# Optimization experiments

Hardware: AMD Instinct MI355X
Metric: run time of the kernel (lower is better)

The kernel has to match this reference:

```python
import jax, jax.numpy as jnp
import numpy as np

N = 16384   # nodes
D = 64      # feature dim
K = 20      # neighbors (self.k)
CHUNK = 2048  # row tile size (mirrors KeOps tiling; avoids n x n materialization)


def setup_inputs() -> dict:
    key = jax.random.key(0)
    k1, = jax.random.split(key, 1)
    x = jax.random.normal(k1, (N, D), dtype=jnp.float32)
    A = jnp.zeros((1,), dtype=jnp.int32)  # unused: embed_f is identity
    temperature = jnp.asarray(4.0, dtype=jnp.float32)  # nn.Parameter init for euclidean
    return {"x": x, "A": A, "temperature": temperature}


def reference(x, A, temperature):
    # embed_f = identity -> x stays [n, d]; batch dim b=1 added at the end
    n, d = x.shape
    scale = jnp.exp(jnp.clip(temperature, -5.0, 5.0))
    sq = jnp.sum(x * x, axis=-1)  # [n]

    def chunk_knn(xc):  # xc: [CHUNK, d]
        # squared euclidean distances of chunk rows vs all points: [CHUNK, n]
        d2 = jnp.sum(xc * xc, axis=-1, keepdims=True) + sq[None, :] - 2.0 * (xc @ x.T)
        # argKmin over j of d2 * scale  (scale > 0 so ordering matches original)
        _, idx = jax.lax.top_k(-(d2 * scale), K)
        return idx  # [CHUNK, K]

    idx = jax.lax.map(chunk_knn, x.reshape(n // CHUNK, CHUNK, d)).reshape(n, K)

    # gather neighbors and recompute logprobs exactly as the torch gather path
    x1 = x[idx]                                  # [n, K, d]
    d2 = jnp.sum((x1 - x[:, None, :]) ** 2, -1)  # [n, K]
    logprobs = (-d2 * scale)[None]               # [1, n, K]

    rows = jnp.broadcast_to(jnp.arange(n)[:, None], (n, K)).reshape(-1)
    # sparse=True, b=1: offset arange(b)*n == 0, final shape [2, b*n*k]
    edges = jnp.stack((idx.reshape(-1), rows), axis=0)  # [2, n*K]

    return (x[None], edges, logprobs)
```

## Files before the change

kernel.cpp:

```cpp
#include <hip/hip_runtime.h>
#include <math.h>

#define NN 16384
#define DD 64
#define KK 20
#define SAMP_CH 16
#define SAMP_PER 32
#define SAMP_N 512
#define THR_EPS 1e-3f
#define BF16_MARGIN 0.25f
#define FCH 4
#define SLOTS 128
#define CAP2 512
#define GS 2

#define SCALE_ULP_NUDGE (+1)

typedef __attribute__((ext_vector_type(8)))  short bf16x8;
typedef __attribute__((ext_vector_type(16))) float f32x16;

__device__ __forceinline__ float nudge_ulp(float v, int n) {
    return __uint_as_float(__float_as_uint(v) + (unsigned)n);
}

__device__ __forceinline__ unsigned short f2bf(float f) {
    unsigned u = __float_as_uint(f);
    return (unsigned short)((u + 0x7fffu + ((u >> 16) & 1u)) >> 16);
}

__device__ __forceinline__ unsigned ordmap(float f) {
    unsigned u = __float_as_uint(f);
    return u ^ ((u & 0x80000000u) ? 0xFFFFFFFFu : 0x80000000u);
}

__device__ __forceinline__ float fast_key(const float* __restrict__ xj4,
                                          const float* xi, float sqj) {
    const float4* xj = reinterpret_cast<const float4*>(xj4);
    float c0 = 0.f, c1 = 0.f, c2 = 0.f, c3 = 0.f;
#pragma unroll
    for (int q = 0; q < 16; ++q) {
        float4 v = xj[q];
        c0 = fmaf(xi[4 * q + 0], v.x, c0);
        c1 = fmaf(xi[4 * q + 1], v.y, c1);
        c2 = fmaf(xi[4 * q + 2], v.z, c2);
        c3 = fmaf(xi[4 * q + 3], v.w, c3);
    }
    return sqj - 2.0f * ((c0 + c1) + (c2 + c3));
}

__device__ __forceinline__ float ref_key(const float* __restrict__ xj4,
                                         const float* xi, float sqi, float sqj,
                                         float scale) {
    const float4* xj = reinterpret_cast<const float4*>(xj4);
    float c = 0.0f;
#pragma unroll
    for (int q = 0; q < 16; ++q) {
        float4 v = xj[q];
        c = fmaf(xi[4 * q + 0], v.x, c);
        c = fmaf(xi[4 * q + 1], v.y, c);
        c = fmaf(xi[4 * q + 2], v.z, c);
        c = fmaf(xi[4 * q + 3], v.w, c);
    }
    float t1 = sqi + sqj;
    float d2 = fmaf(-2.0f, c, t1);
    return d2 * scale;
}

__device__ __forceinline__ float gather_d2(const float* xi,
                                           const float* __restrict__ xj4) {
#pragma clang fp contract(off)
    const float4* xn = reinterpret_cast<const float4*>(xj4);
    float r0, r1, r2, r3, r4, r5, r6, r7;
    {
        float4 v0 = xn[0], v1 = xn[1];
        float d0 = xi[0] - v0.x, d1 = xi[1] - v0.y, d2 = xi[2] - v0.z, d3 = xi[3] - v0.w;
        float d4 = xi[4] - v1.x, d5 = xi[5] - v1.y, d6 = xi[6] - v1.z, d7 = xi[7] - v1.w;
        r0 = d0 * d0; r1 = d1 * d1; r2 = d2 * d2; r3 = d3 * d3;
        r4 = d4 * d4; r5 = d5 * d5; r6 = d6 * d6; r7 = d7 * d7;
    }
#pragma unroll
    for (int t = 1; t < 8; ++t) {
        float4 v0 = xn[2 * t], v1 = xn[2 * t + 1];
        float d0 = xi[8 * t + 0] - v0.x, d1 = xi[8 * t + 1] - v0.y;
        float d2 = xi[8 * t + 2] - v0.z, d3 = xi[8 * t + 3] - v0.w;
        float d4 = xi[8 * t + 4] - v1.x, d5 = xi[8 * t + 5] - v1.y;
        float d6 = xi[8 * t + 6] - v1.z, d7 = xi[8 * t + 7] - v1.w;
        r0 += d0 * d0; r1 += d1 * d1; r2 += d2 * d2; r3 += d3 * d3;
        r4 += d4 * d4; r5 += d5 * d5; r6 += d6 * d6; r7 += d7 * d7;
    }
    return ((r0 + r1) + (r2 + r3)) + ((r4 + r5) + (r6 + r7));
}

__global__ __launch_bounds__(256) void copy_x_kernel(const float* __restrict__ x,
                                                     float* __restrict__ out_x,
                                                     unsigned short* __restrict__ xb) {
    int t = blockIdx.x * blockDim.x + threadIdx.x;
    float4 v = reinterpret_cast<const float4*>(x)[t];
    reinterpret_cast<float4*>(out_x)[t] = v;
    ushort4 w;
    w.x = f2bf(v.x); w.y = f2bf(v.y); w.z = f2bf(v.z); w.w = f2bf(v.w);
    reinterpret_cast<ushort4*>(xb)[t] = w;
}

__global__ __launch_bounds__(256, 2) void sq_kernel(const float* __restrict__ x,
                                                    float* __restrict__ sq) {
#pragma clang fp contract(off)
    int r = blockIdx.x * blockDim.x + threadIdx.x;
    const float4* p = reinterpret_cast<const float4*>(x + (size_t)r * DD);
    float r0, r1, r2, r3, r4, r5, r6, r7;
    {
        float4 v0 = p[0], v1 = p[1];
        r0 = v0.x * v0.x; r1 = v0.y * v0.y; r2 = v0.z * v0.z; r3 = v0.w * v0.w;
        r4 = v1.x * v1.x; r5 = v1.y * v1.y; r6 = v1.z * v1.z; r7 = v1.w * v1.w;
    }
#pragma unroll
    for (int t = 1; t < 8; ++t) {
        float4 v0 = p[2 * t], v1 = p[2 * t + 1];
        r0 += v0.x * v0.x; r1 += v0.y * v0.y; r2 += v0.z * v0.z; r3 += v0.w * v0.w;
        r4 += v1.x * v1.x; r5 += v1.y * v1.y; r6 += v1.z * v1.z; r7 += v1.w * v1.w;
    }
    sq[r] = ((r0 + r1) + (r2 + r3)) + ((r4 + r5) + (r6 + r7));
}

__global__ __launch_bounds__(256, 2) void sample_kernel(const float* __restrict__ x,
                                                        const float* __restrict__ sq,
                                                        float* __restrict__ psum,
                                                        float* __restrict__ psumsq) {
    int g = blockIdx.x * blockDim.x + threadIdx.x;
    int i = g & (NN - 1);
    int c = g >> 14;

    float xi[DD];
#pragma unroll
    for (int d = 0; d < DD; d += 4) {
        float4 v = *reinterpret_cast<const float4*>(x + (size_t)i * DD + d);
        xi[d + 0] = v.x; xi[d + 1] = v.y; xi[d + 2] = v.z; xi[d + 3] = v.w;
    }

    float s = 0.0f, ss = 0.0f;
#pragma unroll 2
    for (int t = 0; t < SAMP_PER; ++t) {
        int j = ((c * SAMP_PER + t) << 5);
        float key = fast_key(x + (size_t)j * DD, xi, sq[j]);
        s += key;
        ss = fmaf(key, key, ss);
    }
    psum[i * SAMP_CH + c]   = s;
    psumsq[i * SAMP_CH + c] = ss;
}

__global__ __launch_bounds__(256) void thr_kernel(const float* __restrict__ psum,
                                                  const float* __restrict__ psumsq,
                                                  const float* __restrict__ sq,
                                                  float* __restrict__ thr) {
    int i = blockIdx.x * blockDim.x + threadIdx.x;
    float S = 0.0f, SS = 0.0f;
#pragma unroll
    for (int c = 0; c < SAMP_CH; ++c) {
        S  += psum[i * SAMP_CH + c];
        SS += psumsq[i * SAMP_CH + c];
    }
    float mean = S * (1.0f / SAMP_N);
    float var  = fmaxf(SS * (1.0f / SAMP_N) - mean * mean, 1.0f);
    float sig  = sqrtf(var);
    float sqi  = sq[i];
    float t2   = 2.0f * (64.0f + 2.0f * sqi);
    float gam  = 8.0f * (64.0f + 3.0f * sqi) / (t2 * sqrtf(t2));
    const float zt = 2.25f;
    float zeff = zt - gam * (zt * zt - 1.0f) * (1.0f / 6.0f);
    thr[i] = mean - zeff * sig + THR_EPS;
}

__global__ __launch_bounds__(256, 2) void filter_mfma_kernel(
    const unsigned short* __restrict__ xb, const float* __restrict__ sq,
    const float* __restrict__ thr, unsigned short* __restrict__ cnt2d,
    unsigned short* __restrict__ surv2d) {
    __shared__ __align__(16) unsigned short lbuf[32][SLOTS];
    __shared__ int lcnt[32];

    const int wave = threadIdx.x >> 6;
    const int lane = threadIdx.x & 63;
    const int bi = blockIdx.x >> 2;
    const int bj = blockIdx.x & 3;
    const int i0 = bi * 32;
    const int jw0 = bj * 4096 + wave * 1024;

    const int arow = i0 + (lane & 31);
    const int koff = (lane >> 5) * 8;

    bf16x8 a[4];
#pragma unroll
    for (int q = 0; q < 4; ++q)
        a[q] = *reinterpret_cast<const bf16x8*>(xb + (size_t)arow * DD + koff + 16 * q);

    float thrv[16];
#pragma unroll
    for (int r = 0; r < 16; ++r) {
        int row = i0 + (r & 3) + 8 * (r >> 2) + 4 * (lane >> 5);
        thrv[r] = thr[row] + BF16_MARGIN;
    }

    if (threadIdx.x < 32) lcnt[threadIdx.x] = 0;
    __syncthreads();

    for (int t = 0; t < 32; ++t) {
        const int j0 = jw0 + t * 32;
        const int jcol = j0 + (lane & 31);
        bf16x8 b[4];
#pragma unroll
        for (int q = 0; q < 4; ++q)
            b[q] = *reinterpret_cast<const bf16x8*>(xb + (size_t)jcol * DD + koff + 16 * q);

        f32x16 acc;
#pragma unroll
        for (int r = 0; r < 16; ++r) acc[r] = 0.0f;
#pragma unroll
        for (int q = 0; q < 4; ++q)
            acc = __builtin_amdgcn_mfma_f32_32x32x16_bf16(a[q], b[q], acc, 0, 0, 0);

        const float sqj = sq[jcol];
#pragma unroll
        for (int r = 0; r < 16; ++r) {
            float key = fmaf(-2.0f, acc[r], sqj);
            if (key <= thrv[r]) {
                int rl = (r & 3) + 8 * (r >> 2) + 4 * (lane >> 5);
                int pos = atomicAdd(&lcnt[rl], 1);
                if (pos < SLOTS) lbuf[rl][pos] = (unsigned short)jcol;
            }
        }
    }
    __syncthreads();

    if (threadIdx.x < 32) {
        int c = lcnt[threadIdx.x];
        cnt2d[(size_t)(i0 + threadIdx.x) * FCH + bj] =
            (unsigned short)(c > 255 ? 255 : c);
    }
#pragma unroll
    for (int z = 0; z < 2; ++z) {
        int idx = threadIdx.x * 2 + z;
        int rl = idx >> 4;
        int sb = (idx & 15) * 8;
        uint4 v = *reinterpret_cast<const uint4*>(&lbuf[rl][sb]);
        *reinterpret_cast<uint4*>(
            &surv2d[((size_t)(i0 + rl) * FCH + bj) * SLOTS + sb]) = v;
    }
}

__global__ __launch_bounds__(256) void flag_kernel(
    const unsigned short* __restrict__ cnt2d, unsigned short* __restrict__ flags) {
    int i = blockIdx.x * blockDim.x + threadIdx.x;
    int mx = 0, tot = 0;
#pragma unroll
    for (int c = 0; c < FCH; ++c) {
        int v = (int)cnt2d[(size_t)i * FCH + c];
        mx = max(mx, v);
        tot += v;
    }
    flags[i] = (mx > SLOTS || tot < KK) ? (unsigned short)0xFFFF
                                        : (unsigned short)tot;
}

__global__ __launch_bounds__(256, 2) void score_rank_out_kernel(
    const float* __restrict__ x, const float* __restrict__ sq,
    const unsigned short* __restrict__ cnt2d,
    const unsigned short* __restrict__ surv2d,
    const unsigned short* __restrict__ flags,
    const float* __restrict__ temp,
    float* __restrict__ out_idx, float* __restrict__ out_rows,
    float* __restrict__ out_lp) {
    __shared__ __align__(16) unsigned long long comp[CAP2];
    __shared__ float xi_lds[DD];
    __shared__ int cbase[FCH + 1];
    const int p = threadIdx.x;

    float tc = fminf(fmaxf(temp[0], -5.0f), 5.0f);
    float scale = nudge_ulp((float)exp((double)tc), SCALE_ULP_NUDGE);

    for (int it = 0; it < GS; ++it) {
        const int i = blockIdx.x * GS + it;
        if (flags[i] == 0xFFFF) continue;

        if (p < 16) {
            float4 v = *reinterpret_cast<const float4*>(x + (size_t)i * DD + 4 * p);
            xi_lds[4 * p + 0] = v.x; xi_lds[4 * p + 1] = v.y;
            xi_lds[4 * p + 2] = v.z; xi_lds[4 * p + 3] = v.w;
        }
        if (p == 0) {
            int run = 0;
#pragma unroll
            for (int c = 0; c < FCH; ++c) {
                cbase[c] = run;
                run += (int)cnt2d[(size_t)i * FCH + c];
            }
            cbase[FCH] = run;
        }
        __syncthreads();

        const float sqi = sq[i];
        const int tot = cbase[FCH];
        int jdx0 = 0x7fffffff, jdx1 = 0x7fffffff;
        unsigned long long my0 = 0xFFFFFFFFFFFFFFFFull;
        unsigned long long my1 = 0xFFFFFFFFFFFFFFFFull;
        if (p < tot) {
            int c = (p >= cbase[1]) + (p >= cbase[2]) + (p >= cbase[3]);
            int l = p - cbase[c];
            jdx0 = (int)surv2d[((size_t)i * FCH + c) * SLOTS + l];
            float key = ref_key(x + (size_t)jdx0 * DD, xi_lds, sqi, sq[jdx0], scale);
            my0 = ((unsigned long long)ordmap(key) << 32) | (unsigned)jdx0;
        }
        comp[p] = my0;
        {
            int d1 = p + 256;
            if (d1 < tot) {
                int c = (d1 >= cbase[1]) + (d1 >= cbase[2]) + (d1 >= cbase[3]);
                int l = d1 - cbase[c];
                jdx1 = (int)surv2d[((size_t)i * FCH + c) * SLOTS + l];
                float key = ref_key(x + (size_t)jdx1 * DD, xi_lds, sqi, sq[jdx1], scale);
                my1 = ((unsigned long long)ordmap(key) << 32) | (unsigned)jdx1;
            }
            comp[d1] = my1;
        }
        __syncthreads();

        const int nR = (tot + 7) & ~7;
        const ulonglong2* c2 = reinterpret_cast<const ulonglong2*>(comp);
        if (p < tot) {
            int rank = 0;
            for (int q = 0; q < nR; q += 8) {
                ulonglong2 a0 = c2[(q >> 1) + 0];
                ulonglong2 a1 = c2[(q >> 1) + 1];
                ulonglong2 a2 = c2[(q >> 1) + 2];
                ulonglong2 a3 = c2[(q >> 1) + 3];
                rank += (a0.x < my0) + (a0.y < my0) + (a1.x < my0) + (a1.y < my0) +
                        (a2.x < my0) + (a2.y < my0) + (a3.x < my0) + (a3.y < my0);
            }
            if (rank < KK) {
                float d2g = gather_d2(xi_lds, x + (size_t)jdx0 * DD);
                out_idx[i * KK + rank]  = (float)jdx0;
                out_rows[i * KK + rank] = (float)i;
                out_lp[i * KK + rank]   = -(d2g * scale);
            }
        }
        if (jdx1 != 0x7fffffff) {
            int rank = 0;
            for (int q = 0; q < nR; q += 8) {
                ulonglong2 a0 = c2[(q >> 1) + 0];
                ulonglong2 a1 = c2[(q >> 1) + 1];
                ulonglong2 a2 = c2[(q >> 1) + 2];
                ulonglong2 a3 = c2[(q >> 1) + 3];
                rank += (a0.x < my1) + (a0.y < my1) + (a1.x < my1) + (a1.y < my1) +
                        (a2.x < my1) + (a2.y < my1) + (a3.x < my1) + (a3.y < my1);
            }
            if (rank < KK) {
                float d2g = gather_d2(xi_lds, x + (size_t)jdx1 * DD);
                out_idx[i * KK + rank]  = (float)jdx1;
                out_rows[i * KK + rank] = (float)i;
                out_lp[i * KK + rank]   = -(d2g * scale);
            }
        }
        __syncthreads();
    }
}

__global__ __launch_bounds__(256) void backstop_kernel(
    const float* __restrict__ x, const float* __restrict__ sq,
    const unsigned short* __restrict__ flags,
    const float* __restrict__ temp,
    float* __restrict__ out_idx, float* __restrict__ out_rows,
    float* __restrict__ out_lp) {
    const int wave = threadIdx.x >> 6;
    const int lane = threadIdx.x & 63;
    const int i = blockIdx.x * 4 + wave;
    if (flags[i] != 0xFFFF) return;

    float tc = fminf(fmaxf(temp[0], -5.0f), 5.0f);
    float scale = nudge_ulp((float)exp((double)tc), SCALE_ULP_NUDGE);

    float xi[DD];
#pragma unroll
    for (int d = 0; d < DD; d += 4) {
        float4 v = *reinterpret_cast<const float4*>(x + (size_t)i * DD + d);
        xi[d + 0] = v.x; xi[d + 1] = v.y; xi[d + 2] = v.z; xi[d + 3] = v.w;
    }
    const float sqi = sq[i];
    float fk[KK];
    int   fi[KK];
#pragma unroll
    for (int s = 0; s < KK; ++s) { fk[s] = INFINITY; fi[s] = 0x7fffffff; }
    float curMax = INFINITY;
    for (int t = 0; t < NN / 64; ++t) {
        int j = t * 64 + lane;
        float key = fast_key(x + (size_t)j * DD, xi, sq[j]);
        if (key < curMax) {
            bool done = false;
#pragma unroll
            for (int s = 0; s < KK; ++s) {
                bool take = (!done) && (fk[s] == curMax);
                fk[s] = take ? key : fk[s];
                fi[s] = take ? j : fi[s];
                done = done || take;
            }
            float m = fk[0];
#pragma unroll
            for (int s = 1; s < KK; ++s) m = fmaxf(m, fk[s]);
            curMax = m;
        }
    }
    float rk[KK];
#pragma unroll
    for (int s = 0; s < KK; ++s) {
        if (fi[s] != 0x7fffffff)
            rk[s] = ref_key(x + (size_t)fi[s] * DD, xi, sqi, sq[fi[s]], scale);
        else
            rk[s] = INFINITY;
    }
    int wIdx = 0;
    for (int k = 0; k < KK; ++k) {
        float bk = rk[0]; int bi = fi[0];
#pragma unroll
        for (int s = 1; s < KK; ++s)
            if (rk[s] < bk || (rk[s] == bk && fi[s] < bi)) { bk = rk[s]; bi = fi[s]; }
#pragma unroll
        for (int s = 1; s < 64; s <<= 1) {
            float ok = __shfl_xor(bk, s);
            int   oi = __shfl_xor(bi, s);
            if (ok < bk || (ok == bk && oi < bi)) { bk = ok; bi = oi; }
        }
        if (lane == k) wIdx = bi;
#pragma unroll
        for (int s = 0; s < KK; ++s)
            if (fi[s] == bi) rk[s] = INFINITY;
    }

    if (lane < KK) {
        float d2g = gather_d2(xi, x + (size_t)wIdx * DD);
        out_idx[i * KK + lane]  = (float)wIdx;
        out_rows[i * KK + lane] = (float)i;
        out_lp[i * KK + lane]   = -(d2g * scale);
    }
}

extern "C" void kernel_launch(void* const* d_in, const int* in_sizes, int n_in,
                              void* d_out, int out_size, void* d_ws, size_t ws_size,
                              hipStream_t stream) {
    const float* x    = (const float*)d_in[0];
    const float* temp = (const float*)d_in[2];

    float* out = (float*)d_out;
    float* out_x    = out;
    float* out_idx  = out + (size_t)NN * DD;
    float* out_rows = out_idx + (size_t)NN * KK;
    float* out_lp   = out_rows + (size_t)NN * KK;

    float* sq    = (float*)d_ws;
    float* thr   = sq + NN;
    unsigned short* cnt2d  = (unsigned short*)(thr + NN);
    unsigned short* surv2d = cnt2d + (size_t)NN * FCH;
    unsigned short* xb     = surv2d + (size_t)NN * FCH * SLOTS;
    unsigned short* flags  = xb + (size_t)NN * DD;
    float* psum   = (float*)surv2d;
    float* psumsq = psum + (size_t)NN * SAMP_CH;

    copy_x_kernel<<<(NN * DD / 4) / 256, 256, 0, stream>>>(x, out_x, xb);
    sq_kernel<<<NN / 256, 256, 0, stream>>>(x, sq);
    sample_kernel<<<(NN * SAMP_CH) / 256, 256, 0, stream>>>(x, sq, psum, psumsq);
    thr_kernel<<<NN / 256, 256, 0, stream>>>(psum, psumsq, sq, thr);
    filter_mfma_kernel<<<512 * 4, 256, 0, stream>>>(xb, sq, thr, cnt2d, surv2d);
    flag_kernel<<<NN / 256, 256, 0, stream>>>(cnt2d, flags);
    score_rank_out_kernel<<<NN / GS, 256, 0, stream>>>(x, sq, cnt2d, surv2d, flags,
                                                       temp, out_idx, out_rows, out_lp);
    backstop_kernel<<<NN / 4, 256, 0, stream>>>(x, sq, flags, temp,
                                                out_idx, out_rows, out_lp);
}
```

Before: 392.8 us.

## Process one row per block and score two adjacent candidates per thread

The score/rank kernel now launches one block per row instead of looping over two rows per block, which removes a barrier and an early-continue path. Each thread now handles two adjacent candidates (2p and 2p+1). It computes both dot products in one interleaved loop for more instruction-level parallelism, and both ranks in a single pass over the LDS comparison array. The call to ref_key is replaced by inline fmaf arithmetic, so keys may round differently from the previous helper. That could change tie ordering if ref_key was written to match the reference exactly.

After: 506.8 us. 29.0% more time.

```diff
diff --git a/kernel.cpp b/kernel.cpp
--- a/kernel.cpp
+++ b/kernel.cpp
@@ -12,7 +12,6 @@
 #define FCH 4
 #define SLOTS 128
 #define CAP2 512
-#define GS 2
 
 #define SCALE_ULP_NUDGE (+1)
 
@@ -273,93 +272,99 @@
     __shared__ float xi_lds[DD];
     __shared__ int cbase[FCH + 1];
     const int p = threadIdx.x;
+    const int i = blockIdx.x;
+    if (flags[i] == 0xFFFF) return;
 
     float tc = fminf(fmaxf(temp[0], -5.0f), 5.0f);
     float scale = nudge_ulp((float)exp((double)tc), SCALE_ULP_NUDGE);
 
-    for (int it = 0; it < GS; ++it) {
-        const int i = blockIdx.x * GS + it;
-        if (flags[i] == 0xFFFF) continue;
-
-        if (p < 16) {
-            float4 v = *reinterpret_cast<const float4*>(x + (size_t)i * DD + 4 * p);
-            xi_lds[4 * p + 0] = v.x; xi_lds[4 * p + 1] = v.y;
-            xi_lds[4 * p + 2] = v.z; xi_lds[4 * p + 3] = v.w;
-        }
-        if (p == 0) {
-            int run = 0;
-#pragma unroll
-            for (int c = 0; c < FCH; ++c) {
-                cbase[c] = run;
-                run += (int)cnt2d[(size_t)i * FCH + c];
-            }
-            cbase[FCH] = run;
-        }
-        __syncthreads();
-
-        const float sqi = sq[i];
-        const int tot = cbase[FCH];
-        int jdx0 = 0x7fffffff, jdx1 = 0x7fffffff;
-        unsigned long long my0 = 0xFFFFFFFFFFFFFFFFull;
-        unsigned long long my1 = 0xFFFFFFFFFFFFFFFFull;
-        if (p < tot) {
-            int c = (p >= cbase[1]) + (p >= cbase[2]) + (p >= cbase[3]);
-            int l = p - cbase[c];
-            jdx0 = (int)surv2d[((size_t)i * FCH + c) * SLOTS + l];
-            float key = ref_key(x + (size_t)jdx0 * DD, xi_lds, sqi, sq[jdx0], scale);
-            my0 = ((unsigned long long)ordmap(key) << 32) | (unsigned)jdx0;
-        }
-        comp[p] = my0;
-        {
-            int d1 = p + 256;
-            if (d1 < tot) {
-                int c = (d1 >= cbase[1]) + (d1 >= cbase[2]) + (d1 >= cbase[3]);
-                int l = d1 - cbase[c];
-                jdx1 = (int)surv2d[((size_t)i * FCH + c) * SLOTS + l];
-                float key = ref_key(x + (size_t)jdx1 * DD, xi_lds, sqi, sq[jdx1], scale);
-                my1 = ((unsigned long long)ordmap(key) << 32) | (unsigned)jdx1;
-            }
-            comp[d1] = my1;
-        }
-        __syncthreads();
-
+    if (p < 16) {
+        float4 v = *reinterpret_cast<const float4*>(x + (size_t)i * DD + 4 * p);
+        xi_lds[4 * p + 0] = v.x; xi_lds[4 * p + 1] = v.y;
+        xi_lds[4 * p + 2] = v.z; xi_lds[4 * p + 3] = v.w;
+    }
+    if (p == 0) {
+        int run = 0;
+#pragma unroll
+        for (int c = 0; c < FCH; ++c) {
+            cbase[c] = run;
+            run += (int)cnt2d[(size_t)i * FCH + c];
+        }
+        cbase[FCH] = run;
+    }
+    __syncthreads();
+
+    const float sqi = sq[i];
+    const int tot = cbase[FCH];
+    const int d0 = 2 * p, d1 = 2 * p + 1;
+    const bool aA = (d0 < tot), aB = (d1 < tot);
+    int jA = 0, jB = 0;
+    if (aA) {
+        int c = (d0 >= cbase[1]) + (d0 >= cbase[2]) + (d0 >= cbase[3]);
+        jA = (int)surv2d[((size_t)i * FCH + c) * SLOTS + (d0 - cbase[c])];
+    }
+    if (aB) {
+        int c = (d1 >= cbase[1]) + (d1 >= cbase[2]) + (d1 >= cbase[3]);
+        jB = (int)surv2d[((size_t)i * FCH + c) * SLOTS + (d1 - cbase[c])];
+    }
+    unsigned long long myA = 0xFFFFFFFFFFFFFFFFull;
+    unsigned long long myB = 0xFFFFFFFFFFFFFFFFull;
+    if (aA || aB) {
+        const float4* pa = reinterpret_cast<const float4*>(x + (size_t)jA * DD);
+        const float4* pb = reinterpret_cast<const float4*>(x + (size_t)jB * DD);
+        float ca = 0.0f, cb = 0.0f;
+#pragma unroll
+        for (int q = 0; q < 16; ++q) {
+            float4 va = pa[q];
+            float4 vb = pb[q];
+            float w0 = xi_lds[4 * q + 0], w1 = xi_lds[4 * q + 1];
+            float w2 = xi_lds[4 * q + 2], w3 = xi_lds[4 * q + 3];
+            ca = fmaf(w0, va.x, ca);  cb = fmaf(w0, vb.x, cb);
+            ca = fmaf(w1, va.y, ca);  cb = fmaf(w1, vb.y, cb);
+            ca = fmaf(w2, va.z, ca);  cb = fmaf(w2, vb.z, cb);
+            ca = fmaf(w3, va.w, ca);  cb = fmaf(w3, vb.w, cb);
+        }
+        if (aA) {
+            float t1 = sqi + sq[jA];
+            float key = fmaf(-2.0f, ca, t1) * scale;
+            myA = ((unsigned long long)ordmap(key) << 32) | (unsigned)jA;
+        }
+        if (aB) {
+            float t1 = sqi + sq[jB];
+            float key = fmaf(-2.0f, cb, t1) * scale;
+            myB = ((unsigned long long)ordmap(key) << 32) | (unsigned)jB;
+        }
+    }
+    comp[d0] = myA;
+    comp[d1] = myB;
+    __syncthreads();
+
+    if (aA) {
         const int nR = (tot + 7) & ~7;
         const ulonglong2* c2 = reinterpret_cast<const ulonglong2*>(comp);
-        if (p < tot) {
-            int rank = 0;
-            for (int q = 0; q < nR; q += 8) {
-                ulonglong2 a0 = c2[(q >> 1) + 0];
-                ulonglong2 a1 = c2[(q >> 1) + 1];
-                ulonglong2 a2 = c2[(q >> 1) + 2];
-                ulonglong2 a3 = c2[(q >> 1) + 3];
-                rank += (a0.x < my0) + (a0.y < my0) + (a1.x < my0) + (a1.y < my0) +
-                        (a2.x < my0) + (a2.y < my0) + (a3.x < my0) + (a3.y < my0);
-            }
-            if (rank < KK) {
-                float d2g = gather_d2(xi_lds, x + (size_t)jdx0 * DD);
-                out_idx[i * KK + rank]  = (float)jdx0;
-                out_rows[i * KK + rank] = (float)i;
-                out_lp[i * KK + rank]   = -(d2g * scale);
-            }
-        }
-        if (jdx1 != 0x7fffffff) {
-            int rank = 0;
-            for (int q = 0; q < nR; q += 8) {
-                ulonglong2 a0 = c2[(q >> 1) + 0];
-                ulonglong2 a1 = c2[(q >> 1) + 1];
-                ulonglong2 a2 = c2[(q >> 1) + 2];
-                ulonglong2 a3 = c2[(q >> 1) + 3];
-                rank += (a0.x < my1) + (a0.y < my1) + (a1.x < my1) + (a1.y < my1) +
-                        (a2.x < my1) + (a2.y < my1) + (a3.x < my1) + (a3.y < my1);
-            }
-            if (rank < KK) {
-                float d2g = gather_d2(xi_lds, x + (size_t)jdx1 * DD);
-                out_idx[i * KK + rank]  = (float)jdx1;
-                out_rows[i * KK + rank] = (float)i;
-                out_lp[i * KK + rank]   = -(d2g * scale);
-            }
-        }
-        __syncthreads();
+        int rankA = 0, rankB = 0;
+        for (int q = 0; q < nR; q += 8) {
+            ulonglong2 a0 = c2[(q >> 1) + 0];
+            ulonglong2 a1 = c2[(q >> 1) + 1];
+            ulonglong2 a2 = c2[(q >> 1) + 2];
+            ulonglong2 a3 = c2[(q >> 1) + 3];
+            rankA += (a0.x < myA) + (a0.y < myA) + (a1.x < myA) + (a1.y < myA) +
+                     (a2.x < myA) + (a2.y < myA) + (a3.x < myA) + (a3.y < myA);
+            rankB += (a0.x < myB) + (a0.y < myB) + (a1.x < myB) + (a1.y < myB) +
+                     (a2.x < myB) + (a2.y < myB) + (a3.x < myB) + (a3.y < myB);
+        }
+        if (rankA < KK) {
+            float d2g = gather_d2(xi_lds, x + (size_t)jA * DD);
+            out_idx[i * KK + rankA]  = (float)jA;
+            out_rows[i * KK + rankA] = (float)i;
+            out_lp[i * KK + rankA]   = -(d2g * scale);
+        }
+        if (aB && rankB < KK) {
+            float d2g = gather_d2(xi_lds, x + (size_t)jB * DD);
+            out_idx[i * KK + rankB]  = (float)jB;
+            out_rows[i * KK + rankB] = (float)i;
+            out_lp[i * KK + rankB]   = -(d2g * scale);
+        }
     }
 }
 
@@ -468,8 +473,8 @@
     thr_kernel<<<NN / 256, 256, 0, stream>>>(psum, psumsq, sq, thr);
     filter_mfma_kernel<<<512 * 4, 256, 0, stream>>>(xb, sq, thr, cnt2d, surv2d);
     flag_kernel<<<NN / 256, 256, 0, stream>>>(cnt2d, flags);
-    score_rank_out_kernel<<<NN / GS, 256, 0, stream>>>(x, sq, cnt2d, surv2d, flags,
-                                                       temp, out_idx, out_rows, out_lp);
+    score_rank_out_kernel<<<NN, 256, 0, stream>>>(x, sq, cnt2d, surv2d, flags,
+                                                  temp, out_idx, out_rows, out_lp);
     backstop_kernel<<<NN / 4, 256, 0, stream>>>(x, sq, flags, temp,
                                                 out_idx, out_rows, out_lp);
 }
```
